# Performance work log

Hardware: AMD Instinct MI355X
Metric: run time of the kernel (lower is better)

The kernel has to match this reference:

```python
import jax, jax.numpy as jnp
import numpy as np

NUM_HEADS = 16
NUM_KV_HEADS = 4
HEAD_DIM = 128
EPS = 1e-6


def _rotate_half(x):
    x1, x2 = jnp.split(x, 2, axis=-1)
    return jnp.concatenate((-x2, x1), axis=-1)


def _rms_norm(x, w):
    var = jnp.mean(x * x, axis=-1, keepdims=True)
    return x * jax.lax.rsqrt(var + EPS) * w


def setup_inputs() -> dict:
    key = jax.random.key(0)
    ks = jax.random.split(key, 6)
    B, S, H = 2, 2048, 2048
    hidden_states = jax.random.normal(ks[0], (B, S, H), dtype=jnp.float32)
    # real RoPE tables (HF-style: freqs tiled twice along last dim)
    inv_freq = 1.0 / (10000.0 ** (np.arange(0, HEAD_DIM, 2, dtype=np.float32) / HEAD_DIM))
    pos = np.arange(S, dtype=np.float32)
    ang = np.concatenate([pos[:, None] * inv_freq[None, :]] * 2, axis=-1)  # [S, head_dim]
    cos = jnp.broadcast_to(jnp.cos(ang)[None], (B, S, HEAD_DIM)).astype(jnp.float32)
    sin = jnp.broadcast_to(jnp.sin(ang)[None], (B, S, HEAD_DIM)).astype(jnp.float32)
    sc = 0.02
    Wq = jax.random.normal(ks[1], (NUM_HEADS * HEAD_DIM, H), dtype=jnp.float32) * sc
    Wk = jax.random.normal(ks[2], (NUM_KV_HEADS * HEAD_DIM, H), dtype=jnp.float32) * sc
    Wv = jax.random.normal(ks[3], (NUM_KV_HEADS * HEAD_DIM, H), dtype=jnp.float32) * sc
    Wo = jax.random.normal(ks[4], (H, NUM_HEADS * HEAD_DIM), dtype=jnp.float32) * sc
    q_norm_w = jnp.ones((HEAD_DIM,), dtype=jnp.float32)
    k_norm_w = jnp.ones((HEAD_DIM,), dtype=jnp.float32)
    return {"hidden_states": hidden_states, "cos": cos, "sin": sin,
            "Wq": Wq, "Wk": Wk, "Wv": Wv, "Wo": Wo,
            "q_norm_w": q_norm_w, "k_norm_w": k_norm_w}


def reference(hidden_states, cos, sin, Wq, Wk, Wv, Wo, q_norm_w, k_norm_w):
    B, S, H = hidden_states.shape
    groups = NUM_HEADS // NUM_KV_HEADS
    # projections (Linear: x @ W^T), then [B, h, S, d]
    q = (hidden_states @ Wq.T).reshape(B, S, NUM_HEADS, HEAD_DIM).transpose(0, 2, 1, 3)
    k = (hidden_states @ Wk.T).reshape(B, S, NUM_KV_HEADS, HEAD_DIM).transpose(0, 2, 1, 3)
    v = (hidden_states @ Wv.T).reshape(B, S, NUM_KV_HEADS, HEAD_DIM).transpose(0, 2, 1, 3)
    # per-head RMSNorm
    q = _rms_norm(q, q_norm_w)
    k = _rms_norm(k, k_norm_w)
    # RoPE, cos/sin broadcast over heads (unsqueeze_dim=1)
    c = cos[:, None, :, :]
    s = sin[:, None, :, :]
    q = q * c + _rotate_half(q) * s
    k = k * c + _rotate_half(k) * s
    # GQA: expand kv heads
    k = jnp.repeat(k, groups, axis=1)
    v = jnp.repeat(v, groups, axis=1)
    scale = 1.0 / jnp.sqrt(jnp.float32(HEAD_DIM))
    scores = jnp.einsum('bhqd,bhkd->bhqk', q, k) * scale
    attn = jax.nn.softmax(scores, axis=-1)
    out = jnp.einsum('bhqk,bhkd->bhqd', attn, v)
    out = out.transpose(0, 2, 1, 3).reshape(B, S, NUM_HEADS * HEAD_DIM)
    return out @ Wo.T
```

## Files before the change

### kernel.cpp

```cpp
#include <hip/hip_runtime.h>
#include <hip/hip_bf16.h>
#include <stdint.h>

typedef __attribute__((ext_vector_type(8))) short short8;
typedef __attribute__((ext_vector_type(4))) float floatx4;
typedef __attribute__((ext_vector_type(16))) float floatx16;

#define MFMA16(a, b, c) __builtin_amdgcn_mfma_f32_16x16x32_bf16(a, b, c, 0, 0, 0)
#define MFMA32(a, b, c) __builtin_amdgcn_mfma_f32_32x32x16_bf16(a, b, c, 0, 0, 0)

static __device__ __forceinline__ void gload_lds16(const __hip_bfloat16* g, __hip_bfloat16* l) {
  __builtin_amdgcn_global_load_lds(
      (const __attribute__((address_space(1))) void*)g,
      (__attribute__((address_space(3))) void*)l,
      16, 0, 0);
}

__global__ __launch_bounds__(256)
void f2bf_all(const float* __restrict__ h, const float* __restrict__ wq,
              const float* __restrict__ wk, const float* __restrict__ wv,
              const float* __restrict__ wo, __hip_bfloat16* __restrict__ hb,
              __hip_bfloat16* __restrict__ wqkv, __hip_bfloat16* __restrict__ wob) {
  const int blk = blockIdx.x;
  const float* src;
  __hip_bfloat16* dst;
  int off;
  if (blk < 8192)       { src = h;  dst = hb;                          off = blk; }
  else if (blk < 12288) { src = wq; dst = wqkv;                        off = blk - 8192; }
  else if (blk < 13312) { src = wk; dst = wqkv + (size_t)2048 * 2048;  off = blk - 12288; }
  else if (blk < 14336) { src = wv; dst = wqkv + (size_t)2560 * 2048;  off = blk - 13312; }
  else                  { src = wo; dst = wob;                         off = blk - 14336; }
  const int i = off * 1024 + threadIdx.x * 4;
  const float4 v = *(const float4*)(src + i);
  __hip_bfloat16 t[4] = {__float2bfloat16(v.x), __float2bfloat16(v.y),
                         __float2bfloat16(v.z), __float2bfloat16(v.w)};
  *(short4*)(dst + i) = *(const short4*)t;
}

template <typename OUT_T>
__global__ __launch_bounds__(256)
void gemm_bt(const __hip_bfloat16* __restrict__ A, const __hip_bfloat16* __restrict__ Bt,
             OUT_T* __restrict__ C, int M, int N, int K) {
  __shared__ __hip_bfloat16 As[2][128 * 32];
  __shared__ __hip_bfloat16 Bs[2][128 * 32];
  const int tid = threadIdx.x;
  const int wid = tid >> 6, lane = tid & 63;
  const int lg = lane >> 4, lr = lane & 15;
  const int wr = wid >> 1, wc = wid & 1;
  const int m0 = blockIdx.x * 128, n0 = blockIdx.y * 128;
  const int nk = K >> 5;

  floatx4 acc[4][4];
#pragma unroll
  for (int mi = 0; mi < 4; ++mi)
#pragma unroll
    for (int ni = 0; ni < 4; ++ni) acc[mi][ni] = (floatx4)(0.0f);

  auto stage = [&](int buf, int kt) {
    const int k0 = kt << 5;
#pragma unroll
    for (int i = 0; i < 2; ++i) {
      const int e = (i * 256 + tid) * 8;
      const int row = e >> 5, col = e & 31;
      gload_lds16(A + (size_t)(m0 + row) * K + k0 + col, &As[buf][e]);
    }
#pragma unroll
    for (int i = 0; i < 2; ++i) {
      const int e = (i * 256 + tid) * 8;
      const int row = e >> 5, col = e & 31;
      gload_lds16(Bt + (size_t)(n0 + row) * K + k0 + col, &Bs[buf][e]);
    }
  };

  stage(0, 0);
  __syncthreads();

  for (int kt = 0; kt < nk; ++kt) {
    const int cur = kt & 1;
    if (kt + 1 < nk) stage(cur ^ 1, kt + 1);
    short8 af[4], bfr[4];
#pragma unroll
    for (int mi = 0; mi < 4; ++mi)
      af[mi] = *(const short8*)&As[cur][(wr * 64 + mi * 16 + lr) * 32 + lg * 8];
#pragma unroll
    for (int ni = 0; ni < 4; ++ni)
      bfr[ni] = *(const short8*)&Bs[cur][(wc * 64 + ni * 16 + lr) * 32 + lg * 8];
#pragma unroll
    for (int mi = 0; mi < 4; ++mi)
#pragma unroll
      for (int ni = 0; ni < 4; ++ni) acc[mi][ni] = MFMA16(af[mi], bfr[ni], acc[mi][ni]);
    __syncthreads();
  }

#pragma unroll
  for (int mi = 0; mi < 4; ++mi)
#pragma unroll
    for (int ni = 0; ni < 4; ++ni) {
      const int row = m0 + wr * 64 + mi * 16 + lg * 4;
      const int col = n0 + wc * 64 + ni * 16 + lr;
#pragma unroll
      for (int r = 0; r < 4; ++r) {
        C[(size_t)(row + r) * N + col] = (OUT_T)acc[mi][ni][r];
      }
    }
}

__global__ __launch_bounds__(256)
void normrope(const __hip_bfloat16* __restrict__ qkv, const float* __restrict__ cosb,
              const float* __restrict__ sinb, const float* __restrict__ qw,
              const float* __restrict__ kw, __hip_bfloat16* __restrict__ Q,
              __hip_bfloat16* __restrict__ Kblk) {
  const int m = blockIdx.x;
  const int b = m >> 11, s = m & 2047;
  const int wid = threadIdx.x >> 6, lane = threadIdx.x & 63;
  const size_t qkvrow = (size_t)m * 3072;
  const float c1 = cosb[(size_t)m * 128 + lane], s1 = sinb[(size_t)m * 128 + lane];
  const float c2 = cosb[(size_t)m * 128 + lane + 64], s2 = sinb[(size_t)m * 128 + lane + 64];
  const float QS = 0.12753102497113446f;
  for (int h = wid * 5; h < wid * 5 + 5; ++h) {
    const float x1 = __bfloat162float(qkv[qkvrow + h * 128 + lane]);
    const float x2 = __bfloat162float(qkv[qkvrow + h * 128 + lane + 64]);
    float ss = x1 * x1 + x2 * x2;
    ss += __shfl_xor(ss, 1);  ss += __shfl_xor(ss, 2);  ss += __shfl_xor(ss, 4);
    ss += __shfl_xor(ss, 8);  ss += __shfl_xor(ss, 16); ss += __shfl_xor(ss, 32);
    const float rs = rsqrtf(ss * (1.0f / 128.0f) + 1e-6f);
    const float* w = (h < 16) ? qw : kw;
    const float n1 = x1 * rs * w[lane], n2 = x2 * rs * w[lane + 64];
    const float o1 = n1 * c1 - n2 * s1;
    const float o2 = n2 * c2 + n1 * s2;
    if (h < 16) {
      const size_t base = ((size_t)(b * 16 + h) * 2048 + s) * 128;
      Q[base + lane] = __float2bfloat16(o1 * QS);
      Q[base + lane + 64] = __float2bfloat16(o2 * QS);
    } else {
      const int z = b * 4 + (h - 16);
      const int t = s >> 5, kv = s & 31;
      const size_t base =
          (size_t)z * 262144 + t * 4096 + (lane >> 3) * 256 + kv * 8 + (lane & 7);
      Kblk[base] = __float2bfloat16(o1);
      Kblk[base + 2048] = __float2bfloat16(o2);
    }
  }
}

__global__ __launch_bounds__(256)
void vtrans2(const __hip_bfloat16* __restrict__ qkv, __hip_bfloat16* __restrict__ Vt2) {
  __shared__ short L[64 * 65];
  const int tid = threadIdx.x;
  const int t = blockIdx.x, d0 = blockIdx.y * 64, z = blockIdx.z;
  const int b = z >> 2, hkv = z & 3;
  const int s0 = t * 64;
#pragma unroll
  for (int i = 0; i < 2; ++i) {
    const int slot = i * 256 + tid;
    const int srow = slot >> 3, c8 = (slot & 7) * 8;
    const short8 v = *(const short8*)((const short*)qkv +
        (size_t)(b * 2048 + s0 + srow) * 3072 + 2560 + hkv * 128 + d0 + c8);
#pragma unroll
    for (int j = 0; j < 8; ++j) L[(c8 + j) * 65 + srow] = v[j];
  }
  __syncthreads();
  short* dst = (short*)Vt2 + (size_t)z * 262144 + t * 8192;
#pragma unroll
  for (int i = 0; i < 2; ++i) {
    const int slot = i * 256 + tid;
    const int drow = slot >> 3, sc8 = (slot & 7) * 8;
    short8 o;
#pragma unroll
    for (int j = 0; j < 8; ++j) {
      const int p = sc8 + j;
      const int pb = p & 31;
      const int phys = (pb & 3) + ((pb >> 2) & 1) * 8 + ((pb >> 3) & 1) * 4 + (pb & 16);
      o[j] = L[drow * 65 + (p & 32) + phys];
    }
    const int addr = (sc8 >> 5) * 4096 + ((sc8 & 31) >> 3) * 1024 + (d0 + drow) * 8;
    *(short8*)&dst[addr] = o;
  }
}

__global__ __launch_bounds__(512, 4)
void fattn(const __hip_bfloat16* __restrict__ Qg, const __hip_bfloat16* __restrict__ Kb2,
           const __hip_bfloat16* __restrict__ Vt2, __hip_bfloat16* __restrict__ Og) {
  __shared__ short SMEM[35328];

  const int tid = threadIdx.x, wid = tid >> 6, lane = tid & 63;
  const int l31 = lane & 31, hi = lane >> 5;
  const int half = wid >> 2, wq = wid & 3;
  const int qt = blockIdx.x, bh = blockIdx.y;
  const int b = bh >> 4, h = bh & 15, hkv = h >> 2;
  const int z = b * 4 + hkv;
  const int q0w = qt * 128 + wq * 32;

  const __hip_bfloat16* Qrow = Qg + ((size_t)((b * 16 + h) * 2048 + q0w + l31)) * 128;
  short8 qf2[8];
#pragma unroll
  for (int ks = 0; ks < 8; ++ks) qf2[ks] = *(const short8*)(Qrow + ks * 16 + hi * 8);

  const short* Kbase = (const short*)Kb2 + (size_t)z * 262144;
  const short* Vbase = (const short*)Vt2 + (size_t)z * 262144;

  auto stage = [&](int buf, int t) {
    const int gt = half * 32 + t;
    const short* ks = Kbase + gt * 4096 + wq * 1024 + lane * 8;
    const short* vs = Vbase + gt * 4096 + wq * 1024 + lane * 8;
    short* kd = &SMEM[(half * 2 + buf) * 4096 + wq * 1024];
    short* vd = &SMEM[16384 + (half * 2 + buf) * 4096 + wq * 1024];
    gload_lds16((const __hip_bfloat16*)ks, (__hip_bfloat16*)kd);
    gload_lds16((const __hip_bfloat16*)(ks + 512), (__hip_bfloat16*)(kd + 512));
    gload_lds16((const __hip_bfloat16*)vs, (__hip_bfloat16*)vd);
    gload_lds16((const __hip_bfloat16*)(vs + 512), (__hip_bfloat16*)(vd + 512));
  };

  floatx16 oacc[4];
#pragma unroll
  for (int dblk = 0; dblk < 4; ++dblk) oacc[dblk] = (floatx16)(0.0f);
  float la0 = 0.0f, la1 = 0.0f;

  stage(0, 0);
  asm volatile("s_waitcnt vmcnt(0)" ::: "memory");
  __builtin_amdgcn_s_barrier();
  __builtin_amdgcn_sched_barrier(0);

  for (int t = 0; t < 32; ++t) {
    const int cur = t & 1;
    if (t + 1 < 32) stage(cur ^ 1, t + 1);
    const short* Kt = &SMEM[(half * 2 + cur) * 4096];
    const short* Vt = &SMEM[16384 + (half * 2 + cur) * 4096];

    floatx16 st = (floatx16)(0.0f);
    __builtin_amdgcn_s_setprio(1);
#pragma unroll
    for (int ks = 0; ks < 8; ++ks) {
      const short8 kf = *(const short8*)&Kt[(2 * ks + hi) * 256 + l31 * 8];
      st = MFMA32(kf, qf2[ks], st);
    }
    __builtin_amdgcn_s_setprio(0);

    int pk[8];
#pragma unroll
    for (int m = 0; m < 8; ++m) {
      const float e0 = exp2f(st[2 * m]);
      const float e1 = exp2f(st[2 * m + 1]);
      if (m & 1) la1 += e0 + e1; else la0 += e0 + e1;
      asm("v_cvt_pk_bf16_f32 %0, %1, %2" : "=v"(pk[m]) : "v"(e0), "v"(e1));
    }

#pragma unroll
    for (int s = 0; s < 2; ++s) {
      union { int i[4]; short8 s8; } u;
      u.i[0] = pk[4 * s + 0];
      u.i[1] = pk[4 * s + 1];
      u.i[2] = pk[4 * s + 2];
      u.i[3] = pk[4 * s + 3];
      const short8 pB = u.s8;
      const int c = s * 2 + hi;
      __builtin_amdgcn_s_setprio(1);
#pragma unroll
      for (int dblk = 0; dblk < 4; ++dblk) {
        const short8 vf = *(const short8*)&Vt[c * 1024 + dblk * 256 + l31 * 8];
        oacc[dblk] = MFMA32(vf, pB, oacc[dblk]);
      }
      __builtin_amdgcn_s_setprio(0);
    }

    asm volatile("s_waitcnt vmcnt(0)" ::: "memory");
    __builtin_amdgcn_s_barrier();
    __builtin_amdgcn_sched_barrier(0);
  }

  float* fw = (float*)&SMEM[0];
  if (half == 1) {
    float* r = fw + wq * 4416;
#pragma unroll
    for (int dblk = 0; dblk < 4; ++dblk)
#pragma unroll
      for (int a = 0; a < 4; ++a) {
        floatx4 p;
#pragma unroll
        for (int j = 0; j < 4; ++j) p[j] = oacc[dblk][4 * a + j];
        *(floatx4*)&r[lane * 69 + dblk * 16 + a * 4] = p;
      }
    r[lane * 69 + 64] = la0 + la1;
  }
  asm volatile("s_waitcnt lgkmcnt(0)" ::: "memory");
  __builtin_amdgcn_s_barrier();

  float l_own = 0.0f;
  if (half == 0) {
    const float* r = fw + wq * 4416;
#pragma unroll
    for (int dblk = 0; dblk < 4; ++dblk)
#pragma unroll
      for (int a = 0; a < 4; ++a) {
        const floatx4 p = *(const floatx4*)&r[lane * 69 + dblk * 16 + a * 4];
#pragma unroll
        for (int j = 0; j < 4; ++j) oacc[dblk][4 * a + j] += p[j];
      }
    l_own = la0 + la1 + r[lane * 69 + 64];
  }
  asm volatile("s_waitcnt lgkmcnt(0)" ::: "memory");
  __builtin_amdgcn_s_barrier();

  if (half == 0) {
    const float l = l_own + __shfl_xor(l_own, 32);
    const float inv = 1.0f / l;
    short* tw = &SMEM[wid * 4352];
#pragma unroll
    for (int dblk = 0; dblk < 4; ++dblk)
#pragma unroll
      for (int a = 0; a < 4; ++a) {
        __hip_bfloat16 o4[4];
#pragma unroll
        for (int r = 0; r < 4; ++r) o4[r] = __float2bfloat16(oacc[dblk][4 * a + r] * inv);
        *(short4*)&tw[l31 * 136 + dblk * 32 + a * 8 + hi * 4] = *(const short4*)o4;
      }
    __hip_bfloat16* orow =
        Og + ((size_t)(b * 2048 + q0w + (lane >> 1))) * 2048 + h * 128 + (lane & 1) * 64;
    const short* trow = &tw[(lane >> 1) * 136 + (lane & 1) * 64];
#pragma unroll
    for (int c = 0; c < 8; ++c) {
      *(short8*)(orow + c * 8) = *(const short8*)(trow + c * 8);
    }
  }
}

extern "C" void kernel_launch(void* const* d_in, const int* in_sizes, int n_in,
                              void* d_out, int out_size, void* d_ws, size_t ws_size,
                              hipStream_t stream) {
  const float* hidden = (const float*)d_in[0];
  const float* cosb = (const float*)d_in[1];
  const float* sinb = (const float*)d_in[2];
  const float* Wq = (const float*)d_in[3];
  const float* Wk = (const float*)d_in[4];
  const float* Wv = (const float*)d_in[5];
  const float* Wo = (const float*)d_in[6];
  const float* qw = (const float*)d_in[7];
  const float* kw = (const float*)d_in[8];

  char* ws = (char*)d_ws;
  __hip_bfloat16* hidden_bf = (__hip_bfloat16*)ws; ws += (size_t)4096 * 2048 * 2;
  __hip_bfloat16* wqkv = (__hip_bfloat16*)ws;      ws += (size_t)3072 * 2048 * 2;
  __hip_bfloat16* wo_bf = (__hip_bfloat16*)ws;     ws += (size_t)2048 * 2048 * 2;
  __hip_bfloat16* qkv = (__hip_bfloat16*)ws;       ws += (size_t)4096 * 3072 * 2;
  __hip_bfloat16* Qb = (__hip_bfloat16*)ws;        ws += (size_t)2 * 16 * 2048 * 128 * 2;
  __hip_bfloat16* Kblk = (__hip_bfloat16*)ws;      ws += (size_t)2 * 4 * 2048 * 128 * 2;
  __hip_bfloat16* attn = (__hip_bfloat16*)ws;      ws += (size_t)4096 * 2048 * 2;
  __hip_bfloat16* Vt2 = wqkv;

  f2bf_all<<<18432, 256, 0, stream>>>(hidden, Wq, Wk, Wv, Wo, hidden_bf, wqkv, wo_bf);

  gemm_bt<__hip_bfloat16><<<dim3(32, 24), 256, 0, stream>>>(hidden_bf, wqkv, qkv, 4096, 3072, 2048);
  normrope<<<4096, 256, 0, stream>>>(qkv, cosb, sinb, qw, kw, Qb, Kblk);
  vtrans2<<<dim3(32, 2, 8), 256, 0, stream>>>(qkv, Vt2);
  fattn<<<dim3(16, 32), 512, 0, stream>>>(Qb, Kblk, Vt2, attn);
  gemm_bt<float><<<dim3(32, 16), 256, 0, stream>>>(attn, wo_bf, (float*)d_out, 4096, 2048, 2048);
}
```

Before: 256.7 us.

## Drop split-KV halves in attention and software-pipeline QK/exp/PV across tiles

```diff
diff --git a/kernel.cpp b/kernel.cpp
--- a/kernel.cpp
+++ b/kernel.cpp
@@ -178,18 +178,17 @@
   }
 }
 
-__global__ __launch_bounds__(512, 4)
+__global__ __launch_bounds__(256, 3)
 void fattn(const __hip_bfloat16* __restrict__ Qg, const __hip_bfloat16* __restrict__ Kb2,
            const __hip_bfloat16* __restrict__ Vt2, __hip_bfloat16* __restrict__ Og) {
-  __shared__ short SMEM[35328];
+  __shared__ short SMEM[17408];
 
   const int tid = threadIdx.x, wid = tid >> 6, lane = tid & 63;
   const int l31 = lane & 31, hi = lane >> 5;
-  const int half = wid >> 2, wq = wid & 3;
   const int qt = blockIdx.x, bh = blockIdx.y;
   const int b = bh >> 4, h = bh & 15, hkv = h >> 2;
   const int z = b * 4 + hkv;
-  const int q0w = qt * 128 + wq * 32;
+  const int q0w = qt * 128 + wid * 32;
 
   const __hip_bfloat16* Qrow = Qg + ((size_t)((b * 16 + h) * 2048 + q0w + l31)) * 128;
   short8 qf2[8];
@@ -199,16 +198,17 @@
   const short* Kbase = (const short*)Kb2 + (size_t)z * 262144;
   const short* Vbase = (const short*)Vt2 + (size_t)z * 262144;
 
-  auto stage = [&](int buf, int t) {
-    const int gt = half * 32 + t;
-    const short* ks = Kbase + gt * 4096 + wq * 1024 + lane * 8;
-    const short* vs = Vbase + gt * 4096 + wq * 1024 + lane * 8;
-    short* kd = &SMEM[(half * 2 + buf) * 4096 + wq * 1024];
-    short* vd = &SMEM[16384 + (half * 2 + buf) * 4096 + wq * 1024];
+  auto stageK = [&](int buf, int t) {
+    const short* ks = Kbase + t * 4096 + tid * 8;
+    short* kd = &SMEM[buf * 4096 + tid * 8];
     gload_lds16((const __hip_bfloat16*)ks, (__hip_bfloat16*)kd);
-    gload_lds16((const __hip_bfloat16*)(ks + 512), (__hip_bfloat16*)(kd + 512));
+    gload_lds16((const __hip_bfloat16*)(ks + 2048), (__hip_bfloat16*)(kd + 2048));
+  };
+  auto stageV = [&](int buf, int t) {
+    const short* vs = Vbase + t * 4096 + tid * 8;
+    short* vd = &SMEM[8192 + buf * 4096 + tid * 8];
     gload_lds16((const __hip_bfloat16*)vs, (__hip_bfloat16*)vd);
-    gload_lds16((const __hip_bfloat16*)(vs + 512), (__hip_bfloat16*)(vd + 512));
+    gload_lds16((const __hip_bfloat16*)(vs + 2048), (__hip_bfloat16*)(vd + 2048));
   };
 
   floatx16 oacc[4];
@@ -216,18 +216,11 @@
   for (int dblk = 0; dblk < 4; ++dblk) oacc[dblk] = (floatx16)(0.0f);
   float la0 = 0.0f, la1 = 0.0f;
 
-  stage(0, 0);
-  asm volatile("s_waitcnt vmcnt(0)" ::: "memory");
-  __builtin_amdgcn_s_barrier();
-  __builtin_amdgcn_sched_barrier(0);
-
-  for (int t = 0; t < 32; ++t) {
-    const int cur = t & 1;
-    if (t + 1 < 32) stage(cur ^ 1, t + 1);
-    const short* Kt = &SMEM[(half * 2 + cur) * 4096];
-    const short* Vt = &SMEM[16384 + (half * 2 + cur) * 4096];
-
-    floatx16 st = (floatx16)(0.0f);
+  int pkA[8], pkB[8];
+
+  auto doQK = [&](int kbuf, floatx16& st) {
+    const short* Kt = &SMEM[kbuf * 4096];
+    st = (floatx16)(0.0f);
     __builtin_amdgcn_s_setprio(1);
 #pragma unroll
     for (int ks = 0; ks < 8; ++ks) {
@@ -235,8 +228,8 @@
       st = MFMA32(kf, qf2[ks], st);
     }
     __builtin_amdgcn_s_setprio(0);
-
-    int pk[8];
+  };
+  auto doExp = [&](const floatx16& st, int (&pk)[8]) {
 #pragma unroll
     for (int m = 0; m < 8; ++m) {
       const float e0 = exp2f(st[2 * m]);
@@ -244,7 +237,9 @@
       if (m & 1) la1 += e0 + e1; else la0 += e0 + e1;
       asm("v_cvt_pk_bf16_f32 %0, %1, %2" : "=v"(pk[m]) : "v"(e0), "v"(e1));
     }
-
+  };
+  auto doPV = [&](int vbuf, const int (&pk)[8]) {
+    const short* Vt = &SMEM[8192 + vbuf * 4096];
 #pragma unroll
     for (int s = 0; s < 2; ++s) {
       union { int i[4]; short8 s8; } u;
@@ -262,65 +257,64 @@
       }
       __builtin_amdgcn_s_setprio(0);
     }
-
+  };
+
+  auto body = [&](int (&pkPrev)[8], int (&pkCur)[8], int u) {
+    if (u + 1 < 64) stageK((u + 1) & 1, u + 1);
+    stageV(u & 1, u);
+    floatx16 st;
+    doQK(u & 1, st);
+    doPV((u - 1) & 1, pkPrev);
+    doExp(st, pkCur);
     asm volatile("s_waitcnt vmcnt(0)" ::: "memory");
     __builtin_amdgcn_s_barrier();
     __builtin_amdgcn_sched_barrier(0);
-  }
-
-  float* fw = (float*)&SMEM[0];
-  if (half == 1) {
-    float* r = fw + wq * 4416;
-#pragma unroll
-    for (int dblk = 0; dblk < 4; ++dblk)
-#pragma unroll
-      for (int a = 0; a < 4; ++a) {
-        floatx4 p;
-#pragma unroll
-        for (int j = 0; j < 4; ++j) p[j] = oacc[dblk][4 * a + j];
-        *(floatx4*)&r[lane * 69 + dblk * 16 + a * 4] = p;
-      }
-    r[lane * 69 + 64] = la0 + la1;
-  }
+  };
+
+  stageK(0, 0);
+  asm volatile("s_waitcnt vmcnt(0)" ::: "memory");
+  __builtin_amdgcn_s_barrier();
+  __builtin_amdgcn_sched_barrier(0);
+  {
+    stageK(1, 1);
+    stageV(0, 0);
+    floatx16 st;
+    doQK(0, st);
+    doExp(st, pkA);
+    asm volatile("s_waitcnt vmcnt(0)" ::: "memory");
+    __builtin_amdgcn_s_barrier();
+    __builtin_amdgcn_sched_barrier(0);
+  }
+
+  for (int u = 1; u < 63; u += 2) {
+    body(pkA, pkB, u);
+    body(pkB, pkA, u + 1);
+  }
+  body(pkA, pkB, 63);
+  doPV(1, pkB);
+
   asm volatile("s_waitcnt lgkmcnt(0)" ::: "memory");
   __builtin_amdgcn_s_barrier();
 
-  float l_own = 0.0f;
-  if (half == 0) {
-    const float* r = fw + wq * 4416;
-#pragma unroll
-    for (int dblk = 0; dblk < 4; ++dblk)
-#pragma unroll
-      for (int a = 0; a < 4; ++a) {
-        const floatx4 p = *(const floatx4*)&r[lane * 69 + dblk * 16 + a * 4];
-#pragma unroll
-        for (int j = 0; j < 4; ++j) oacc[dblk][4 * a + j] += p[j];
-      }
-    l_own = la0 + la1 + r[lane * 69 + 64];
-  }
-  asm volatile("s_waitcnt lgkmcnt(0)" ::: "memory");
-  __builtin_amdgcn_s_barrier();
-
-  if (half == 0) {
-    const float l = l_own + __shfl_xor(l_own, 32);
-    const float inv = 1.0f / l;
-    short* tw = &SMEM[wid * 4352];
-#pragma unroll
-    for (int dblk = 0; dblk < 4; ++dblk)
-#pragma unroll
-      for (int a = 0; a < 4; ++a) {
-        __hip_bfloat16 o4[4];
-#pragma unroll
-        for (int r = 0; r < 4; ++r) o4[r] = __float2bfloat16(oacc[dblk][4 * a + r] * inv);
-        *(short4*)&tw[l31 * 136 + dblk * 32 + a * 8 + hi * 4] = *(const short4*)o4;
-      }
-    __hip_bfloat16* orow =
-        Og + ((size_t)(b * 2048 + q0w + (lane >> 1))) * 2048 + h * 128 + (lane & 1) * 64;
-    const short* trow = &tw[(lane >> 1) * 136 + (lane & 1) * 64];
-#pragma unroll
-    for (int c = 0; c < 8; ++c) {
-      *(short8*)(orow + c * 8) = *(const short8*)(trow + c * 8);
-    }
+  const float l_own = la0 + la1;
+  const float l = l_own + __shfl_xor(l_own, 32);
+  const float inv = 1.0f / l;
+  short* tw = &SMEM[wid * 4352];
+#pragma unroll
+  for (int dblk = 0; dblk < 4; ++dblk)
+#pragma unroll
+    for (int a = 0; a < 4; ++a) {
+      __hip_bfloat16 o4[4];
+#pragma unroll
+      for (int r = 0; r < 4; ++r) o4[r] = __float2bfloat16(oacc[dblk][4 * a + r] * inv);
+      *(short4*)&tw[l31 * 136 + dblk * 32 + a * 8 + hi * 4] = *(const short4*)o4;
+    }
+  __hip_bfloat16* orow =
+      Og + ((size_t)(b * 2048 + q0w + (lane >> 1))) * 2048 + h * 128 + (lane & 1) * 64;
+  const short* trow = &tw[(lane >> 1) * 136 + (lane & 1) * 64];
+#pragma unroll
+  for (int c = 0; c < 8; ++c) {
+    *(short8*)(orow + c * 8) = *(const short8*)(trow + c * 8);
   }
 }
 
@@ -352,6 +346,6 @@
   gemm_bt<__hip_bfloat16><<<dim3(32, 24), 256, 0, stream>>>(hidden_bf, wqkv, qkv, 4096, 3072, 2048);
   normrope<<<4096, 256, 0, stream>>>(qkv, cosb, sinb, qw, kw, Qb, Kblk);
   vtrans2<<<dim3(32, 2, 8), 256, 0, stream>>>(qkv, Vt2);
-  fattn<<<dim3(16, 32), 512, 0, stream>>>(Qb, Kblk, Vt2, attn);
+  fattn<<<dim3(16, 32), 256, 0, stream>>>(Qb, Kblk, Vt2, attn);
   gemm_bt<float><<<dim3(32, 16), 256, 0, stream>>>(attn, wo_bf, (float*)d_out, 4096, 2048, 2048);
 }
```

Result: faster. 230.7 us (-10.1%).
